# Performance work log

Hardware: AMD Instinct MI355X
Metric: run time of the kernel (lower is better)

Reference implementation:

```python
import jax, jax.numpy as jnp
import numpy as np

N_NODES = 100000
N_EDGES = 1600000
C_IN, C_HID, C_OUT = 64, 64, 32


def _gcn_conv(x, src, dst, ew, W, b, n_nodes):
    """PyG GCNConv: add self-loops (weight 1), symmetric normalization,
    out[dst] += norm * (x @ W)[src], plus bias. Dropout omitted (eval mode)."""
    h = x @ W  # [N, C_out_layer]
    loop = jnp.arange(n_nodes, dtype=src.dtype)
    src_a = jnp.concatenate([src, loop])
    dst_a = jnp.concatenate([dst, loop])
    ew_a = jnp.concatenate([ew, jnp.ones((n_nodes,), dtype=ew.dtype)])
    # degree over incoming (dst) side, weighted
    deg = jax.ops.segment_sum(ew_a, dst_a, num_segments=n_nodes)
    dinv = jnp.where(deg > 0, jax.lax.rsqrt(deg), 0.0)
    norm = dinv[src_a] * ew_a * dinv[dst_a]  # [E+N]
    msg = h[src_a] * norm[:, None]           # gather + scale: [E+N, C]
    out = jax.ops.segment_sum(msg, dst_a, num_segments=n_nodes)  # scatter-add
    return out + b


def setup_inputs() -> dict:
    key = jax.random.key(0)
    k1, k2, k3, k4, k5, k6, k7 = jax.random.split(key, 7)
    x = jax.random.normal(k1, (N_NODES, C_IN), dtype=jnp.float32)
    edge_index = jax.random.randint(k2, (2, N_EDGES), 0, N_NODES, dtype=jnp.int64)
    edge_attr = jax.random.uniform(k3, (N_EDGES,), dtype=jnp.float32)
    s1 = 1.0 / np.sqrt(C_IN)
    s2 = 1.0 / np.sqrt(C_HID)
    W1 = jax.random.uniform(k4, (C_IN, C_HID), jnp.float32, -s1, s1)
    b1 = jnp.zeros((C_HID,), dtype=jnp.float32)
    W2 = jax.random.uniform(k5, (C_HID, C_OUT), jnp.float32, -s2, s2)
    b2 = jnp.zeros((C_OUT,), dtype=jnp.float32)
    return {"x": x, "edge_index": edge_index, "edge_attr": edge_attr,
            "W1": W1, "b1": b1, "W2": W2, "b2": b2}


def reference(x, edge_index, edge_attr, W1, b1, W2, b2):
    n = x.shape[0]
    src, dst = edge_index[0], edge_index[1]
    h = _gcn_conv(x, src, dst, edge_attr, W1, b1, n)
    h = jax.nn.relu(h)  # dropout is identity in eval mode
    out = _gcn_conv(h, src, dst, edge_attr, W2, b2, n)
    return out
```

## Files before the change

kernel.cpp:

```cpp
#include <hip/hip_runtime.h>
#include <hip/hip_fp16.h>


#define TPB 256
#define TPB_P 512
#define TPB_S 512
#define BSH 7
#define BNODES 128
#define PCHUNK 4096
#define CAP 2816

typedef union { uint2 u; __half2 h[2]; } hpack;
typedef union { int4 q; int2 p[2]; } epack;

__global__ __launch_bounds__(256) void k_binit(int* __restrict__ bpos) {
  int i = blockIdx.x * 256 + threadIdx.x;
  if (i < 1024) bpos[i] = i * CAP;
}

__global__ __launch_bounds__(TPB_P) void k_part(const int* __restrict__ si,
                                                const int* __restrict__ di,
                                                const float* __restrict__ ew,
                                                int* __restrict__ bpos,
                                                int2* __restrict__ tin, int e) {
  __shared__ int hcnt[1024];
  __shared__ int hbase[1024];
  int t = threadIdx.x;
  int lo = blockIdx.x * PCHUNK;
  int hi = lo + PCHUNK; if (hi > e) hi = e;
  for (int i = t; i < 1024; i += TPB_P) hcnt[i] = 0;
  __syncthreads();
  for (int i = lo + t; i < hi; i += TPB_P) atomicAdd(&hcnt[di[i] >> BSH], 1);
  __syncthreads();
  int rot = blockIdx.x * 331;
  for (int i = t; i < 1024; i += TPB_P) {
    int j = (i + rot) & 1023;
    int c = hcnt[j];
    hbase[j] = c ? atomicAdd(&bpos[j], c) : 0;
    hcnt[j] = 0;
  }
  __syncthreads();
  for (int i = lo + t; i < hi; i += TPB_P) {
    int d = di[i];
    int bk = d >> BSH;
    int loc = atomicAdd(&hcnt[bk], 1);
    tin[hbase[bk] + loc] = make_int2(si[i] | ((d & (BNODES - 1)) << 17),
                                     __float_as_int(ew[i]));
  }
}

__global__ __launch_bounds__(TPB_S) void k_sortb(const int2* __restrict__ tin,
                                                 const int* __restrict__ bpos,
                                                 int2* __restrict__ colpk,
                                                 int2* __restrict__ rowseg,
                                                 float* __restrict__ dinv, int n) {
  __shared__ int cnt[BNODES];
  __shared__ float degw[BNODES];
  __shared__ int cur[BNODES];
  __shared__ int ls[BNODES];
  int b = blockIdx.x, t = threadIdx.x;
  if (t < BNODES) { cnt[t] = 0; degw[t] = 1.0f; }
  __syncthreads();
  int jb = b * CAP, je = bpos[b];
  for (int j = jb + t; j < je; j += TPB_S) {
    int2 p = tin[j];
    int dl = p.x >> 17;
    atomicAdd(&cnt[dl], 1);
    atomicAdd(&degw[dl], __int_as_float(p.y));
  }
  __syncthreads();
  int c = (t < BNODES) ? cnt[t] : 0;
  int c2 = (c + 1) & ~1;
  if (t < BNODES) ls[t] = c2;
  __syncthreads();
  for (int off = 1; off < BNODES; off <<= 1) {
    int u = (t >= off && t < BNODES) ? ls[t - off] : 0;
    __syncthreads();
    if (t < BNODES) ls[t] += u;
    __syncthreads();
  }
  int base = b << BSH;
  if (t < BNODES) {
    int start = jb + ls[t] - c2;
    cur[t] = start;
    int node = base + t;
    if (node < n) {
      rowseg[node] = make_int2(start, start + c2);
      dinv[node] = rsqrtf(degw[t]);
    }
    if (c & 1) colpk[start + c] = make_int2(0, 0);
  }
  __syncthreads();
  for (int j = jb + t; j < je; j += TPB_S) {
    int2 p = tin[j];
    int dl = p.x >> 17;
    int pos = atomicAdd(&cur[dl], 1);
    colpk[pos] = make_int2(p.x & 0x1FFFF, p.y);
  }
}

__global__ __launch_bounds__(TPB) void k_gemm1(const float* __restrict__ x,
                                               const float* __restrict__ W1,
                                               const float* __restrict__ dinv,
                                               __half* __restrict__ g1h, int n) {
  __shared__ float Wl[64 * 64];
  int t = threadIdx.x;
  {
    const float4* W4 = (const float4*)W1;
    float4* Wl4 = (float4*)Wl;
#pragma unroll
    for (int i = 0; i < 4; ++i) Wl4[t + TPB * i] = W4[t + TPB * i];
  }
  __syncthreads();
  int r = blockIdx.x * 16 + (t >> 4);
  if (r >= n) return;
  int c0 = (t & 15) << 2;
  const float4* xr = (const float4*)(x + (size_t)r * 64);
  float ax = 0.f, ay = 0.f, az = 0.f, aw = 0.f;
#pragma unroll
  for (int kk = 0; kk < 16; ++kk) {
    float4 xv = xr[kk];
    const float* w = &Wl[(kk * 4) * 64 + c0];
    float4 w0 = *(const float4*)(w);
    float4 w1 = *(const float4*)(w + 64);
    float4 w2 = *(const float4*)(w + 128);
    float4 w3 = *(const float4*)(w + 192);
    ax += xv.x * w0.x + xv.y * w1.x + xv.z * w2.x + xv.w * w3.x;
    ay += xv.x * w0.y + xv.y * w1.y + xv.z * w2.y + xv.w * w3.y;
    az += xv.x * w0.z + xv.y * w1.z + xv.z * w2.z + xv.w * w3.z;
    aw += xv.x * w0.w + xv.y * w1.w + xv.z * w2.w + xv.w * w3.w;
  }
  float dv = dinv[r];
  hpack pk;
  pk.h[0] = __floats2half2_rn(dv * ax, dv * ay);
  pk.h[1] = __floats2half2_rn(dv * az, dv * aw);
  *(uint2*)(g1h + (size_t)r * 64 + c0) = pk.u;
}

__global__ __launch_bounds__(TPB) void k_gather64(const __half* __restrict__ g1h,
                                                  const int2* __restrict__ colpk,
                                                  const int2* __restrict__ rowseg,
                                                  float* __restrict__ acc, int n) {
  int t = threadIdx.x;
  int r = blockIdx.x * 16 + (t >> 4);
  if (r >= n) return;
  int c0 = (t & 15) << 2;
  hpack s; s.u = *(const uint2*)(g1h + (size_t)r * 64 + c0);
  float2 s01 = __half22float2(s.h[0]), s23 = __half22float2(s.h[1]);
  float ax = s01.x, ay = s01.y, az = s23.x, aw = s23.y;
  int2 seg = rowseg[r];
  int j = seg.x;
  for (; j + 3 < seg.y; j += 4) {
    epack q0; q0.q = *(const int4*)(colpk + j);
    epack q1; q1.q = *(const int4*)(colpk + j + 2);
    float w0 = __int_as_float(q0.p[0].y), w1 = __int_as_float(q0.p[1].y);
    float w2 = __int_as_float(q1.p[0].y), w3 = __int_as_float(q1.p[1].y);
    hpack u0; u0.u = *(const uint2*)(g1h + (size_t)q0.p[0].x * 64 + c0);
    hpack u1; u1.u = *(const uint2*)(g1h + (size_t)q0.p[1].x * 64 + c0);
    hpack u2; u2.u = *(const uint2*)(g1h + (size_t)q1.p[0].x * 64 + c0);
    hpack u3; u3.u = *(const uint2*)(g1h + (size_t)q1.p[1].x * 64 + c0);
    float2 a01 = __half22float2(u0.h[0]), a23 = __half22float2(u0.h[1]);
    float2 b01 = __half22float2(u1.h[0]), b23 = __half22float2(u1.h[1]);
    float2 c01 = __half22float2(u2.h[0]), c23 = __half22float2(u2.h[1]);
    float2 d01 = __half22float2(u3.h[0]), d23 = __half22float2(u3.h[1]);
    ax += w0 * a01.x + w1 * b01.x + w2 * c01.x + w3 * d01.x;
    ay += w0 * a01.y + w1 * b01.y + w2 * c01.y + w3 * d01.y;
    az += w0 * a23.x + w1 * b23.x + w2 * c23.x + w3 * d23.x;
    aw += w0 * a23.y + w1 * b23.y + w2 * c23.y + w3 * d23.y;
  }
  if (j < seg.y) {
    epack q0; q0.q = *(const int4*)(colpk + j);
    float w0 = __int_as_float(q0.p[0].y), w1 = __int_as_float(q0.p[1].y);
    hpack u0; u0.u = *(const uint2*)(g1h + (size_t)q0.p[0].x * 64 + c0);
    hpack u1; u1.u = *(const uint2*)(g1h + (size_t)q0.p[1].x * 64 + c0);
    float2 a01 = __half22float2(u0.h[0]), a23 = __half22float2(u0.h[1]);
    float2 b01 = __half22float2(u1.h[0]), b23 = __half22float2(u1.h[1]);
    ax += w0 * a01.x + w1 * b01.x;
    ay += w0 * a01.y + w1 * b01.y;
    az += w0 * a23.x + w1 * b23.x;
    aw += w0 * a23.y + w1 * b23.y;
  }
  float4 o = {ax, ay, az, aw};
  *(float4*)(acc + (size_t)r * 64 + c0) = o;
}

__global__ __launch_bounds__(TPB) void k_gemm2(const float* __restrict__ acc1,
                                               const float* __restrict__ W2,
                                               const float* __restrict__ b1,
                                               const float* __restrict__ dinv,
                                               __half* __restrict__ g2h, int n) {
  __shared__ float Wl[64 * 32];
  __shared__ float b1l[64];
  int t = threadIdx.x;
  {
    const float4* W4 = (const float4*)W2;
    float4* Wl4 = (float4*)Wl;
#pragma unroll
    for (int i = 0; i < 2; ++i) Wl4[t + TPB * i] = W4[t + TPB * i];
    if (t < 64) b1l[t] = b1[t];
  }
  __syncthreads();
  int r = blockIdx.x * 32 + (t >> 3);
  if (r >= n) return;
  int c0 = (t & 7) << 2;
  float dv = dinv[r];
  const float4* ar = (const float4*)(acc1 + (size_t)r * 64);
  float ax = 0.f, ay = 0.f, az = 0.f, aw = 0.f;
#pragma unroll
  for (int kk = 0; kk < 16; ++kk) {
    float4 v = ar[kk];
    float x0 = fmaxf(dv * v.x + b1l[4 * kk + 0], 0.f);
    float x1 = fmaxf(dv * v.y + b1l[4 * kk + 1], 0.f);
    float x2 = fmaxf(dv * v.z + b1l[4 * kk + 2], 0.f);
    float x3 = fmaxf(dv * v.w + b1l[4 * kk + 3], 0.f);
    const float* w = &Wl[(kk * 4) * 32 + c0];
    float4 w0 = *(const float4*)(w);
    float4 w1 = *(const float4*)(w + 32);
    float4 w2 = *(const float4*)(w + 64);
    float4 w3 = *(const float4*)(w + 96);
    ax += x0 * w0.x + x1 * w1.x + x2 * w2.x + x3 * w3.x;
    ay += x0 * w0.y + x1 * w1.y + x2 * w2.y + x3 * w3.y;
    az += x0 * w0.z + x1 * w1.z + x2 * w2.z + x3 * w3.z;
    aw += x0 * w0.w + x1 * w1.w + x2 * w2.w + x3 * w3.w;
  }
  hpack pk;
  pk.h[0] = __floats2half2_rn(dv * ax, dv * ay);
  pk.h[1] = __floats2half2_rn(dv * az, dv * aw);
  *(uint2*)(g2h + (size_t)r * 32 + c0) = pk.u;
}

__global__ __launch_bounds__(TPB) void k_gather32(const __half* __restrict__ g2h,
                                                  const int2* __restrict__ colpk,
                                                  const int2* __restrict__ rowseg,
                                                  const float* __restrict__ dinv,
                                                  const float* __restrict__ b2,
                                                  float* __restrict__ out, int n) {
  int t = threadIdx.x;
  int r = blockIdx.x * 32 + (t >> 3);
  if (r >= n) return;
  int c0 = (t & 7) << 2;
  hpack s; s.u = *(const uint2*)(g2h + (size_t)r * 32 + c0);
  float2 s01 = __half22float2(s.h[0]), s23 = __half22float2(s.h[1]);
  float ax = s01.x, ay = s01.y, az = s23.x, aw = s23.y;
  int2 seg = rowseg[r];
  int j = seg.x;
  for (; j + 3 < seg.y; j += 4) {
    epack q0; q0.q = *(const int4*)(colpk + j);
    epack q1; q1.q = *(const int4*)(colpk + j + 2);
    float w0 = __int_as_float(q0.p[0].y), w1 = __int_as_float(q0.p[1].y);
    float w2 = __int_as_float(q1.p[0].y), w3 = __int_as_float(q1.p[1].y);
    hpack u0; u0.u = *(const uint2*)(g2h + (size_t)q0.p[0].x * 32 + c0);
    hpack u1; u1.u = *(const uint2*)(g2h + (size_t)q0.p[1].x * 32 + c0);
    hpack u2; u2.u = *(const uint2*)(g2h + (size_t)q1.p[0].x * 32 + c0);
    hpack u3; u3.u = *(const uint2*)(g2h + (size_t)q1.p[1].x * 32 + c0);
    float2 a01 = __half22float2(u0.h[0]), a23 = __half22float2(u0.h[1]);
    float2 b01 = __half22float2(u1.h[0]), b23 = __half22float2(u1.h[1]);
    float2 c01 = __half22float2(u2.h[0]), c23 = __half22float2(u2.h[1]);
    float2 d01 = __half22float2(u3.h[0]), d23 = __half22float2(u3.h[1]);
    ax += w0 * a01.x + w1 * b01.x + w2 * c01.x + w3 * d01.x;
    ay += w0 * a01.y + w1 * b01.y + w2 * c01.y + w3 * d01.y;
    az += w0 * a23.x + w1 * b23.x + w2 * c23.x + w3 * d23.x;
    aw += w0 * a23.y + w1 * b23.y + w2 * c23.y + w3 * d23.y;
  }
  if (j < seg.y) {
    epack q0; q0.q = *(const int4*)(colpk + j);
    float w0 = __int_as_float(q0.p[0].y), w1 = __int_as_float(q0.p[1].y);
    hpack u0; u0.u = *(const uint2*)(g2h + (size_t)q0.p[0].x * 32 + c0);
    hpack u1; u1.u = *(const uint2*)(g2h + (size_t)q0.p[1].x * 32 + c0);
    float2 a01 = __half22float2(u0.h[0]), a23 = __half22float2(u0.h[1]);
    float2 b01 = __half22float2(u1.h[0]), b23 = __half22float2(u1.h[1]);
    ax += w0 * a01.x + w1 * b01.x;
    ay += w0 * a01.y + w1 * b01.y;
    az += w0 * a23.x + w1 * b23.x;
    aw += w0 * a23.y + w1 * b23.y;
  }
  float dv = dinv[r];
  float4 bb = *(const float4*)(b2 + c0);
  float4 o = {dv * ax + bb.x, dv * ay + bb.y, dv * az + bb.z, dv * aw + bb.w};
  *(float4*)(out + (size_t)r * 32 + c0) = o;
}

extern "C" void kernel_launch(void* const* d_in, const int* in_sizes, int n_in,
                              void* d_out, int out_size, void* d_ws, size_t ws_size,
                              hipStream_t stream) {
  const float* x  = (const float*)d_in[0];
  const int* ei   = (const int*)d_in[1];
  const float* ew = (const float*)d_in[2];
  const float* W1 = (const float*)d_in[3];
  const float* b1 = (const float*)d_in[4];
  const float* W2 = (const float*)d_in[5];
  const float* b2 = (const float*)d_in[6];
  float* out = (float*)d_out;

  const int n = in_sizes[0] / 64;
  const int e = in_sizes[1] / 2;
  const int* si = ei;
  const int* di = ei + e;
  const int NB = (n + BNODES - 1) / BNODES;

  float* ws = (float*)d_ws;
  const size_t NP = 100352;
  float*  dinv   = ws;
  __half* g1h    = (__half*)(ws + NP);
  float*  acc1   = ws + NP + (size_t)n * 32;
  int2*   rowseg = (int2*)(acc1 + (size_t)n * 64);
  int*    bpos   = (int*)(rowseg + NP);
  int2*   colpk  = (int2*)(bpos + 1024);
  int2*   tin    = (int2*)acc1;
  __half* g2h    = g1h;

  int gb_part = (e + PCHUNK - 1) / PCHUNK;
  int gb_16 = (n + 15) / 16;
  int gb_32 = (n + 31) / 32;

  k_binit<<<4, 256, 0, stream>>>(bpos);
  k_part<<<gb_part, TPB_P, 0, stream>>>(si, di, ew, bpos, tin, e);
  k_sortb<<<NB, TPB_S, 0, stream>>>(tin, bpos, colpk, rowseg, dinv, n);
  k_gemm1<<<gb_16, TPB, 0, stream>>>(x, W1, dinv, g1h, n);
  k_gather64<<<gb_16, TPB, 0, stream>>>(g1h, colpk, rowseg, acc1, n);
  k_gemm2<<<gb_32, TPB, 0, stream>>>(acc1, W2, b1, dinv, g2h, n);
  k_gather32<<<gb_32, TPB, 0, stream>>>(g2h, colpk, rowseg, dinv, b2, out, n);
}
```

Measured before the change: 230.7 us.

## Coarsen partition buckets, stage partition writes in LDS, unroll gathers by eight

Bucketing in the partition and sort kernels is coarsened from 1024 buckets of 128 nodes to 256 buckets of 512 nodes, and the sort kernel now uses 1024 threads per block. The partition kernel first sorts each chunk's edges by bucket in shared memory, then writes them out contiguously, so global scatter writes coalesce better. Both gather kernels unroll the edge loop to 8 so more loads are in flight. In exchange there are fewer, larger sort blocks, more shared memory use, and higher register pressure in the gathers.

```diff
diff --git a/kernel.cpp b/kernel.cpp
--- a/kernel.cpp
+++ b/kernel.cpp
@@ -4,18 +4,19 @@
 
 #define TPB 256
 #define TPB_P 512
-#define TPB_S 512
-#define BSH 7
-#define BNODES 128
+#define TPB_S 1024
+#define BSH2 9
+#define BN2 512
+#define NBC 256
 #define PCHUNK 4096
-#define CAP 2816
+#define CAP2 9728
 
 typedef union { uint2 u; __half2 h[2]; } hpack;
 typedef union { int4 q; int2 p[2]; } epack;
 
 __global__ __launch_bounds__(256) void k_binit(int* __restrict__ bpos) {
-  int i = blockIdx.x * 256 + threadIdx.x;
-  if (i < 1024) bpos[i] = i * CAP;
+  int i = threadIdx.x;
+  if (i < NBC) bpos[i] = i * CAP2;
 }
 
 __global__ __launch_bounds__(TPB_P) void k_part(const int* __restrict__ si,
@@ -23,29 +24,46 @@
                                                 const float* __restrict__ ew,
                                                 int* __restrict__ bpos,
                                                 int2* __restrict__ tin, int e) {
-  __shared__ int hcnt[1024];
-  __shared__ int hbase[1024];
+  __shared__ int hcnt[NBC];
+  __shared__ int lst0[NBC];
+  __shared__ int lcur[NBC];
+  __shared__ int hbase[NBC];
+  __shared__ int2 se[PCHUNK];
+  __shared__ unsigned char sbk[PCHUNK];
   int t = threadIdx.x;
   int lo = blockIdx.x * PCHUNK;
   int hi = lo + PCHUNK; if (hi > e) hi = e;
-  for (int i = t; i < 1024; i += TPB_P) hcnt[i] = 0;
-  __syncthreads();
-  for (int i = lo + t; i < hi; i += TPB_P) atomicAdd(&hcnt[di[i] >> BSH], 1);
-  __syncthreads();
-  int rot = blockIdx.x * 331;
-  for (int i = t; i < 1024; i += TPB_P) {
-    int j = (i + rot) & 1023;
-    int c = hcnt[j];
-    hbase[j] = c ? atomicAdd(&bpos[j], c) : 0;
-    hcnt[j] = 0;
+  int cn = hi - lo;
+  if (t < NBC) hcnt[t] = 0;
+  __syncthreads();
+  for (int i = lo + t; i < hi; i += TPB_P) atomicAdd(&hcnt[di[i] >> BSH2], 1);
+  __syncthreads();
+  int c = (t < NBC) ? hcnt[t] : 0;
+  for (int off = 1; off < NBC; off <<= 1) {
+    int u = (t >= off && t < NBC) ? hcnt[t - off] : 0;
+    __syncthreads();
+    if (t < NBC) hcnt[t] += u;
+    __syncthreads();
+  }
+  if (t < NBC) {
+    int ex = hcnt[t] - c;
+    lst0[t] = ex;
+    lcur[t] = 0;
+    hbase[t] = c ? atomicAdd(&bpos[t], c) : 0;
   }
   __syncthreads();
   for (int i = lo + t; i < hi; i += TPB_P) {
     int d = di[i];
-    int bk = d >> BSH;
-    int loc = atomicAdd(&hcnt[bk], 1);
-    tin[hbase[bk] + loc] = make_int2(si[i] | ((d & (BNODES - 1)) << 17),
-                                     __float_as_int(ew[i]));
+    int bk = d >> BSH2;
+    int loc = atomicAdd(&lcur[bk], 1);
+    int p = lst0[bk] + loc;
+    se[p] = make_int2(si[i] | ((d & (BN2 - 1)) << 17), __float_as_int(ew[i]));
+    sbk[p] = (unsigned char)bk;
+  }
+  __syncthreads();
+  for (int p = t; p < cn; p += TPB_P) {
+    int bk = sbk[p];
+    tin[hbase[bk] + (p - lst0[bk])] = se[p];
   }
 }
 
@@ -54,14 +72,14 @@
                                                  int2* __restrict__ colpk,
                                                  int2* __restrict__ rowseg,
                                                  float* __restrict__ dinv, int n) {
-  __shared__ int cnt[BNODES];
-  __shared__ float degw[BNODES];
-  __shared__ int cur[BNODES];
-  __shared__ int ls[BNODES];
+  __shared__ int cnt[BN2];
+  __shared__ float degw[BN2];
+  __shared__ int cur[BN2];
+  __shared__ int ls[BN2];
   int b = blockIdx.x, t = threadIdx.x;
-  if (t < BNODES) { cnt[t] = 0; degw[t] = 1.0f; }
-  __syncthreads();
-  int jb = b * CAP, je = bpos[b];
+  if (t < BN2) { cnt[t] = 0; degw[t] = 1.0f; }
+  __syncthreads();
+  int jb = b * CAP2, je = bpos[b];
   for (int j = jb + t; j < je; j += TPB_S) {
     int2 p = tin[j];
     int dl = p.x >> 17;
@@ -69,18 +87,18 @@
     atomicAdd(&degw[dl], __int_as_float(p.y));
   }
   __syncthreads();
-  int c = (t < BNODES) ? cnt[t] : 0;
+  int c = (t < BN2) ? cnt[t] : 0;
   int c2 = (c + 1) & ~1;
-  if (t < BNODES) ls[t] = c2;
-  __syncthreads();
-  for (int off = 1; off < BNODES; off <<= 1) {
-    int u = (t >= off && t < BNODES) ? ls[t - off] : 0;
+  if (t < BN2) ls[t] = c2;
+  __syncthreads();
+  for (int off = 1; off < BN2; off <<= 1) {
+    int u = (t >= off && t < BN2) ? ls[t - off] : 0;
     __syncthreads();
-    if (t < BNODES) ls[t] += u;
+    if (t < BN2) ls[t] += u;
     __syncthreads();
   }
-  int base = b << BSH;
-  if (t < BNODES) {
+  int base = b << BSH2;
+  if (t < BN2) {
     int start = jb + ls[t] - c2;
     cur[t] = start;
     int node = base + t;
@@ -150,25 +168,42 @@
   float ax = s01.x, ay = s01.y, az = s23.x, aw = s23.y;
   int2 seg = rowseg[r];
   int j = seg.x;
-  for (; j + 3 < seg.y; j += 4) {
+  for (; j + 7 < seg.y; j += 8) {
     epack q0; q0.q = *(const int4*)(colpk + j);
     epack q1; q1.q = *(const int4*)(colpk + j + 2);
-    float w0 = __int_as_float(q0.p[0].y), w1 = __int_as_float(q0.p[1].y);
-    float w2 = __int_as_float(q1.p[0].y), w3 = __int_as_float(q1.p[1].y);
+    epack q2; q2.q = *(const int4*)(colpk + j + 4);
+    epack q3; q3.q = *(const int4*)(colpk + j + 6);
     hpack u0; u0.u = *(const uint2*)(g1h + (size_t)q0.p[0].x * 64 + c0);
     hpack u1; u1.u = *(const uint2*)(g1h + (size_t)q0.p[1].x * 64 + c0);
     hpack u2; u2.u = *(const uint2*)(g1h + (size_t)q1.p[0].x * 64 + c0);
     hpack u3; u3.u = *(const uint2*)(g1h + (size_t)q1.p[1].x * 64 + c0);
-    float2 a01 = __half22float2(u0.h[0]), a23 = __half22float2(u0.h[1]);
-    float2 b01 = __half22float2(u1.h[0]), b23 = __half22float2(u1.h[1]);
-    float2 c01 = __half22float2(u2.h[0]), c23 = __half22float2(u2.h[1]);
-    float2 d01 = __half22float2(u3.h[0]), d23 = __half22float2(u3.h[1]);
-    ax += w0 * a01.x + w1 * b01.x + w2 * c01.x + w3 * d01.x;
-    ay += w0 * a01.y + w1 * b01.y + w2 * c01.y + w3 * d01.y;
-    az += w0 * a23.x + w1 * b23.x + w2 * c23.x + w3 * d23.x;
-    aw += w0 * a23.y + w1 * b23.y + w2 * c23.y + w3 * d23.y;
-  }
-  if (j < seg.y) {
+    hpack u4; u4.u = *(const uint2*)(g1h + (size_t)q2.p[0].x * 64 + c0);
+    hpack u5; u5.u = *(const uint2*)(g1h + (size_t)q2.p[1].x * 64 + c0);
+    hpack u6; u6.u = *(const uint2*)(g1h + (size_t)q3.p[0].x * 64 + c0);
+    hpack u7; u7.u = *(const uint2*)(g1h + (size_t)q3.p[1].x * 64 + c0);
+    float w0 = __int_as_float(q0.p[0].y), w1 = __int_as_float(q0.p[1].y);
+    float w2 = __int_as_float(q1.p[0].y), w3 = __int_as_float(q1.p[1].y);
+    float w4 = __int_as_float(q2.p[0].y), w5 = __int_as_float(q2.p[1].y);
+    float w6 = __int_as_float(q3.p[0].y), w7 = __int_as_float(q3.p[1].y);
+    float2 a01, a23;
+    a01 = __half22float2(u0.h[0]); a23 = __half22float2(u0.h[1]);
+    ax += w0 * a01.x; ay += w0 * a01.y; az += w0 * a23.x; aw += w0 * a23.y;
+    a01 = __half22float2(u1.h[0]); a23 = __half22float2(u1.h[1]);
+    ax += w1 * a01.x; ay += w1 * a01.y; az += w1 * a23.x; aw += w1 * a23.y;
+    a01 = __half22float2(u2.h[0]); a23 = __half22float2(u2.h[1]);
+    ax += w2 * a01.x; ay += w2 * a01.y; az += w2 * a23.x; aw += w2 * a23.y;
+    a01 = __half22float2(u3.h[0]); a23 = __half22float2(u3.h[1]);
+    ax += w3 * a01.x; ay += w3 * a01.y; az += w3 * a23.x; aw += w3 * a23.y;
+    a01 = __half22float2(u4.h[0]); a23 = __half22float2(u4.h[1]);
+    ax += w4 * a01.x; ay += w4 * a01.y; az += w4 * a23.x; aw += w4 * a23.y;
+    a01 = __half22float2(u5.h[0]); a23 = __half22float2(u5.h[1]);
+    ax += w5 * a01.x; ay += w5 * a01.y; az += w5 * a23.x; aw += w5 * a23.y;
+    a01 = __half22float2(u6.h[0]); a23 = __half22float2(u6.h[1]);
+    ax += w6 * a01.x; ay += w6 * a01.y; az += w6 * a23.x; aw += w6 * a23.y;
+    a01 = __half22float2(u7.h[0]); a23 = __half22float2(u7.h[1]);
+    ax += w7 * a01.x; ay += w7 * a01.y; az += w7 * a23.x; aw += w7 * a23.y;
+  }
+  for (; j + 1 < seg.y; j += 2) {
     epack q0; q0.q = *(const int4*)(colpk + j);
     float w0 = __int_as_float(q0.p[0].y), w1 = __int_as_float(q0.p[1].y);
     hpack u0; u0.u = *(const uint2*)(g1h + (size_t)q0.p[0].x * 64 + c0);
@@ -244,25 +279,42 @@
   float ax = s01.x, ay = s01.y, az = s23.x, aw = s23.y;
   int2 seg = rowseg[r];
   int j = seg.x;
-  for (; j + 3 < seg.y; j += 4) {
+  for (; j + 7 < seg.y; j += 8) {
     epack q0; q0.q = *(const int4*)(colpk + j);
     epack q1; q1.q = *(const int4*)(colpk + j + 2);
-    float w0 = __int_as_float(q0.p[0].y), w1 = __int_as_float(q0.p[1].y);
-    float w2 = __int_as_float(q1.p[0].y), w3 = __int_as_float(q1.p[1].y);
+    epack q2; q2.q = *(const int4*)(colpk + j + 4);
+    epack q3; q3.q = *(const int4*)(colpk + j + 6);
     hpack u0; u0.u = *(const uint2*)(g2h + (size_t)q0.p[0].x * 32 + c0);
     hpack u1; u1.u = *(const uint2*)(g2h + (size_t)q0.p[1].x * 32 + c0);
     hpack u2; u2.u = *(const uint2*)(g2h + (size_t)q1.p[0].x * 32 + c0);
     hpack u3; u3.u = *(const uint2*)(g2h + (size_t)q1.p[1].x * 32 + c0);
-    float2 a01 = __half22float2(u0.h[0]), a23 = __half22float2(u0.h[1]);
-    float2 b01 = __half22float2(u1.h[0]), b23 = __half22float2(u1.h[1]);
-    float2 c01 = __half22float2(u2.h[0]), c23 = __half22float2(u2.h[1]);
-    float2 d01 = __half22float2(u3.h[0]), d23 = __half22float2(u3.h[1]);
-    ax += w0 * a01.x + w1 * b01.x + w2 * c01.x + w3 * d01.x;
-    ay += w0 * a01.y + w1 * b01.y + w2 * c01.y + w3 * d01.y;
-    az += w0 * a23.x + w1 * b23.x + w2 * c23.x + w3 * d23.x;
-    aw += w0 * a23.y + w1 * b23.y + w2 * c23.y + w3 * d23.y;
-  }
-  if (j < seg.y) {
+    hpack u4; u4.u = *(const uint2*)(g2h + (size_t)q2.p[0].x * 32 + c0);
+    hpack u5; u5.u = *(const uint2*)(g2h + (size_t)q2.p[1].x * 32 + c0);
+    hpack u6; u6.u = *(const uint2*)(g2h + (size_t)q3.p[0].x * 32 + c0);
+    hpack u7; u7.u = *(const uint2*)(g2h + (size_t)q3.p[1].x * 32 + c0);
+    float w0 = __int_as_float(q0.p[0].y), w1 = __int_as_float(q0.p[1].y);
+    float w2 = __int_as_float(q1.p[0].y), w3 = __int_as_float(q1.p[1].y);
+    float w4 = __int_as_float(q2.p[0].y), w5 = __int_as_float(q2.p[1].y);
+    float w6 = __int_as_float(q3.p[0].y), w7 = __int_as_float(q3.p[1].y);
+    float2 a01, a23;
+    a01 = __half22float2(u0.h[0]); a23 = __half22float2(u0.h[1]);
+    ax += w0 * a01.x; ay += w0 * a01.y; az += w0 * a23.x; aw += w0 * a23.y;
+    a01 = __half22float2(u1.h[0]); a23 = __half22float2(u1.h[1]);
+    ax += w1 * a01.x; ay += w1 * a01.y; az += w1 * a23.x; aw += w1 * a23.y;
+    a01 = __half22float2(u2.h[0]); a23 = __half22float2(u2.h[1]);
+    ax += w2 * a01.x; ay += w2 * a01.y; az += w2 * a23.x; aw += w2 * a23.y;
+    a01 = __half22float2(u3.h[0]); a23 = __half22float2(u3.h[1]);
+    ax += w3 * a01.x; ay += w3 * a01.y; az += w3 * a23.x; aw += w3 * a23.y;
+    a01 = __half22float2(u4.h[0]); a23 = __half22float2(u4.h[1]);
+    ax += w4 * a01.x; ay += w4 * a01.y; az += w4 * a23.x; aw += w4 * a23.y;
+    a01 = __half22float2(u5.h[0]); a23 = __half22float2(u5.h[1]);
+    ax += w5 * a01.x; ay += w5 * a01.y; az += w5 * a23.x; aw += w5 * a23.y;
+    a01 = __half22float2(u6.h[0]); a23 = __half22float2(u6.h[1]);
+    ax += w6 * a01.x; ay += w6 * a01.y; az += w6 * a23.x; aw += w6 * a23.y;
+    a01 = __half22float2(u7.h[0]); a23 = __half22float2(u7.h[1]);
+    ax += w7 * a01.x; ay += w7 * a01.y; az += w7 * a23.x; aw += w7 * a23.y;
+  }
+  for (; j + 1 < seg.y; j += 2) {
     epack q0; q0.q = *(const int4*)(colpk + j);
     float w0 = __int_as_float(q0.p[0].y), w1 = __int_as_float(q0.p[1].y);
     hpack u0; u0.u = *(const uint2*)(g2h + (size_t)q0.p[0].x * 32 + c0);
@@ -296,7 +348,7 @@
   const int e = in_sizes[1] / 2;
   const int* si = ei;
   const int* di = ei + e;
-  const int NB = (n + BNODES - 1) / BNODES;
+  const int NBc = (n + BN2 - 1) >> BSH2;
 
   float* ws = (float*)d_ws;
   const size_t NP = 100352;
@@ -313,9 +365,9 @@
   int gb_16 = (n + 15) / 16;
   int gb_32 = (n + 31) / 32;
 
-  k_binit<<<4, 256, 0, stream>>>(bpos);
+  k_binit<<<1, 256, 0, stream>>>(bpos);
   k_part<<<gb_part, TPB_P, 0, stream>>>(si, di, ew, bpos, tin, e);
-  k_sortb<<<NB, TPB_S, 0, stream>>>(tin, bpos, colpk, rowseg, dinv, n);
+  k_sortb<<<NBc, TPB_S, 0, stream>>>(tin, bpos, colpk, rowseg, dinv, n);
   k_gemm1<<<gb_16, TPB, 0, stream>>>(x, W1, dinv, g1h, n);
   k_gather64<<<gb_16, TPB, 0, stream>>>(g1h, colpk, rowseg, acc1, n);
   k_gemm2<<<gb_32, TPB, 0, stream>>>(acc1, W2, b1, dinv, g2h, n);
```

New measurement: 222.4 us. -3.6%, faster.
